# Kernel optimization log

Hardware: AMD Instinct MI355X
Metric: run time of the kernel (lower is better)

The kernel has to match this reference:

```python
import jax, jax.numpy as jnp
import numpy as np

B, S, E, H, R = 512, 50, 128, 8, 32
D = E // H  # depth per head
USERS, ITEMS, ALLSEQ, NCLASS = 50000, 20000, 20000, 5


def setup_inputs() -> dict:
    key = jax.random.key(0)
    ks = jax.random.split(key, 20)
    n = lambda k, shp, s=0.05: jax.random.normal(k, shp, dtype=jnp.float32) * s
    return {
        "user": jax.random.randint(ks[0], (B,), 0, USERS),
        "item": jax.random.randint(ks[1], (B,), 0, ITEMS),
        "neighbor": jax.random.randint(ks[2], (B, S), 0, USERS),
        "seq": jax.random.randint(ks[3], (B, S), 0, ALLSEQ),
        "user_emb_table": n(ks[4], (USERS, E)),
        "item_emb_table": n(ks[5], (ITEMS, E)),
        "user_item_LCU": n(ks[6], (ALLSEQ, R, E), 0.01),
        "item_user_LCU": n(ks[7], (ALLSEQ, R, E), 0.01),
        "wq": n(ks[8], (E, E)), "bq": jnp.zeros((E,), jnp.float32),
        "wk": n(ks[9], (E, E)), "bk": jnp.zeros((E,), jnp.float32),
        "wv": n(ks[10], (E, E)), "bv": jnp.zeros((E,), jnp.float32),
        "wo": n(ks[11], (E, E)), "bo": jnp.zeros((E,), jnp.float32),
        "fc_w": n(ks[12], (R, NCLASS)), "fc_b": jnp.zeros((NCLASS,), jnp.float32),
    }


def _forward(user, item, neighbor, seq,
             user_emb_table, item_emb_table, user_item_LCU, item_user_LCU,
             wq, bq, wk, bk, wv, bv, wo, bo, fc_w, fc_b):
    user_emb = user_emb_table[user]            # [B,E]
    neighbor_emb = user_emb_table[neighbor]    # [B,S,E]
    item_emb = item_emb_table[item]            # [B,E]
    weight = (neighbor > 0).astype(jnp.float32)  # [B,S] padding mask (1=real)

    # ---- single-query multi-head attention (use_attention=True) ----
    q = (user_emb @ wq + bq).reshape(B, H, D)                       # [B,H,D]
    k = (neighbor_emb @ wk + bk).reshape(B, S, H, D).transpose(0, 2, 1, 3)  # [B,H,S,D]
    v = (neighbor_emb @ wv + bv).reshape(B, S, H, D).transpose(0, 2, 1, 3)  # [B,H,S,D]
    logits = jnp.einsum('bhd,bhsd->bhs', q, k) / jnp.sqrt(jnp.float32(D))
    logits = logits + (1.0 - weight)[:, None, :] * (-1e9)           # mask padding
    attn = jax.nn.softmax(logits, axis=-1)                          # [B,H,S]
    ctx = attn[..., None] * v                                       # [B,H,S,D]
    ctx = ctx.transpose(0, 2, 1, 3).reshape(B, S, E)                # [B,S,E]
    neighbor_emb = ctx @ wo + bo                                    # [B,S,E]

    # ---- region embedding ----
    K_ui = user_item_LCU[seq]   # [B,S,R,E]
    K_iu = item_user_LCU[seq]   # [B,S,R,E]
    neighbor_profile = jnp.einsum('bsre,bse->bsr', K_iu, neighbor_emb)  # [B,S,R]
    item_profile = jnp.einsum('bsre,be->bsr', K_ui, item_emb)          # [B,S,R]
    neighbor_rating = neighbor_profile * item_profile * weight[:, :, None]
    user_rating_vector = jnp.max(neighbor_rating, axis=1)              # [B,R]

    # ---- rating classifier ----
    return jax.nn.softmax(user_rating_vector @ fc_w + fc_b, axis=-1)   # [B,NCLASS]


def reference(user, item, neighbor, seq,
              user_emb_table, item_emb_table, user_item_LCU, item_user_LCU,
              wq, bq, wk, bk, wv, bv, wo, bo, fc_w, fc_b):
    return _forward(user, item, neighbor, seq,
                    user_emb_table, item_emb_table, user_item_LCU, item_user_LCU,
                    wq, bq, wk, bk, wv, bv, wo, bo, fc_w, fc_b)
```

## Files before the change

### kernel.cpp

```cpp
#include <hip/hip_runtime.h>
#include <math.h>

#define BB 512
#define SS 50
#define EE 128
#define HH 8
#define RR 32
#define NC 5
#define NSEQ 20000
#define NBS (BB*SS)
#define LDK 136
#define NRB 2048

typedef __attribute__((ext_vector_type(8))) __bf16 bf16x8;
typedef __attribute__((ext_vector_type(4))) float f32x4;
typedef __attribute__((ext_vector_type(4))) unsigned short us4;

__device__ __forceinline__ unsigned short f2bf(float f) {
    unsigned int u = __float_as_uint(f);
    unsigned int r = (u + 0x7fffu + ((u >> 16) & 1u)) >> 16;
    return (unsigned short)r;
}
__device__ __forceinline__ float dot4v(const f32x4& a, const float4& b) {
    return a[0]*b.x + a[1]*b.y + a[2]*b.z + a[3]*b.w;
}

__global__ __launch_bounds__(256) void prep_kernel(const float* __restrict__ wv,
                                                   const float* __restrict__ wo,
                                                   unsigned short* __restrict__ wvT,
                                                   unsigned short* __restrict__ woT,
                                                   const int* __restrict__ seq,
                                                   int* __restrict__ hist) {
    const int bid = blockIdx.x, t = threadIdx.x;
    if (bid < 128) {
        const int n = bid;
        if (t < 128) wvT[n*EE + t] = f2bf(wv[t*EE + n]);
        else         woT[n*EE + (t - 128)] = f2bf(wo[(t - 128)*EE + n]);
    } else {
        const int i = (bid - 128) * 256 + t;
        if (i < NBS) atomicAdd(&hist[seq[i]], 1);
    }
}

__global__ __launch_bounds__(1024) void scan_kernel(int* __restrict__ hist,
                                                    int* __restrict__ jlist,
                                                    int* __restrict__ jstart,
                                                    int* __restrict__ Mcount) {
    const int t = threadIdx.x;
    const int CH = 20;
    const int base = t * CH;
    int val[CH];
    int s = 0, cz = 0;
    #pragma unroll
    for (int i = 0; i < CH; ++i) {
        int idx = base + i;
        int v = (idx < NSEQ) ? hist[idx] : 0;
        val[i] = v;
        s += v;
        cz += (v > 0) ? 1 : 0;
    }
    const int lane = t & 63, w = t >> 6;
    int incl = s, incl2 = cz;
    #pragma unroll
    for (int off = 1; off < 64; off <<= 1) {
        int n1 = __shfl_up(incl, off);
        int n2 = __shfl_up(incl2, off);
        if (lane >= off) { incl += n1; incl2 += n2; }
    }
    __shared__ int wsum[16], wsum2[16];
    if (lane == 63) { wsum[w] = incl; wsum2[w] = incl2; }
    __syncthreads();
    if (t == 0) {
        int a = 0, b = 0;
        #pragma unroll
        for (int k = 0; k < 16; ++k) {
            int v1 = wsum[k], v2 = wsum2[k];
            wsum[k] = a; wsum2[k] = b;
            a += v1; b += v2;
        }
    }
    __syncthreads();
    int e  = incl  - s  + wsum[w];
    int c2 = incl2 - cz + wsum2[w];
    #pragma unroll
    for (int i = 0; i < CH; ++i) {
        int idx = base + i;
        if (idx < NSEQ) {
            hist[idx] = e;
            if (val[i] > 0) { jlist[c2] = idx; jstart[c2] = e; ++c2; }
            e += val[i];
        }
    }
    if (t == 1023) {
        int M = wsum2[15] + incl2;
        Mcount[0] = M;
        jstart[M] = NBS;
    }
}

__global__ __launch_bounds__(256) void scatter_kernel(const int* __restrict__ seq,
                                                      const int* __restrict__ neighbor,
                                                      const int* __restrict__ item,
                                                      int* __restrict__ hist,
                                                      int* __restrict__ pinfo,
                                                      int* __restrict__ pitem) {
    int i = blockIdx.x * 256 + threadIdx.x;
    if (i < NBS) {
        int pos = atomicAdd(&hist[seq[i]], 1);
        pinfo[pos] = i | ((neighbor[i] > 0) ? 0 : 0x80000000);
        pitem[pos] = item[(unsigned)i / SS];
    }
}

__global__ __launch_bounds__(256, 4) void attn_kernel(
    const int* __restrict__ user,
    const int* __restrict__ neighbor,
    const float* __restrict__ uet,
    const float* __restrict__ wq, const float* __restrict__ bq,
    const float* __restrict__ wk, const float* __restrict__ bk,
    const float* __restrict__ bv, const float* __restrict__ bo,
    const unsigned short* __restrict__ wvT, const unsigned short* __restrict__ woT,
    float* __restrict__ ws_ne2)
{
    __shared__ unsigned short kA[64*LDK];
    __shared__ unsigned short qkvT[16][EE];
    __shared__ float ue[EE];
    __shared__ float qs[EE];
    __shared__ float qkb[HH];
    __shared__ float attn_s[HH][64];
    __shared__ float maskadd[64];

    const int b = blockIdx.x;
    const int t = threadIdx.x;

    if (t < EE) ue[t] = uet[(size_t)user[b]*EE + t];
    if (t < 64) maskadd[t] = (t < SS && neighbor[b*SS + t] > 0) ? 0.f : -1e9f;
    for (int idx = t; idx < SS*32; idx += 256) {
        int s = idx >> 5, g = idx & 31;
        float4 v = ((const float4*)(uet + (size_t)neighbor[b*SS + s]*EE))[g];
        us4 o; o.x = f2bf(v.x); o.y = f2bf(v.y); o.z = f2bf(v.z); o.w = f2bf(v.w);
        *(us4*)&kA[s*LDK + g*4] = o;
    }
    for (int idx = t; idx < 14*LDK; idx += 256) kA[50*LDK + idx] = 0;
    for (int idx = t; idx < 8*EE; idx += 256) qkvT[8 + (idx >> 7)][idx & 127] = 0;
    __syncthreads();

    if (t < EE) {
        float acc = bq[t];
        #pragma unroll 4
        for (int e = 0; e < EE; ++e) acc = fmaf(ue[e], wq[e*EE + t], acc);
        qs[t] = acc;
    }
    __syncthreads();

    {
        const int e = t >> 1, h0 = (t & 1) * 4;
        const float* wrow = wk + e*EE;
        #pragma unroll
        for (int j = 0; j < 4; ++j) {
            int h = h0 + j;
            float acc = 0.f;
            #pragma unroll
            for (int d = 0; d < 16; ++d) acc = fmaf(qs[h*16 + d], wrow[h*16 + d], acc);
            qkvT[h][e] = f2bf(acc);
        }
    }
    if (t < HH) {
        float acc = 0.f;
        #pragma unroll
        for (int d = 0; d < 16; ++d) acc = fmaf(qs[t*16 + d], bk[t*16 + d], acc);
        qkb[t] = acc;
    }
    __syncthreads();

    const int w    = t >> 6;
    const int l    = t & 63;
    const int lrow = l & 15;
    const int kg   = l >> 4;

    bf16x8 a0 = *(const bf16x8*)&kA[(w*16 + lrow)*LDK +  0 + kg*8];
    bf16x8 a1 = *(const bf16x8*)&kA[(w*16 + lrow)*LDK + 32 + kg*8];
    bf16x8 a2 = *(const bf16x8*)&kA[(w*16 + lrow)*LDK + 64 + kg*8];
    bf16x8 a3 = *(const bf16x8*)&kA[(w*16 + lrow)*LDK + 96 + kg*8];

    {
        bf16x8 b0 = *(const bf16x8*)&qkvT[lrow][ 0 + kg*8];
        bf16x8 b1 = *(const bf16x8*)&qkvT[lrow][32 + kg*8];
        bf16x8 b2 = *(const bf16x8*)&qkvT[lrow][64 + kg*8];
        bf16x8 b3 = *(const bf16x8*)&qkvT[lrow][96 + kg*8];
        f32x4 c = {0.f, 0.f, 0.f, 0.f};
        c = __builtin_amdgcn_mfma_f32_16x16x32_bf16(a0, b0, c, 0, 0, 0);
        c = __builtin_amdgcn_mfma_f32_16x16x32_bf16(a1, b1, c, 0, 0, 0);
        c = __builtin_amdgcn_mfma_f32_16x16x32_bf16(a2, b2, c, 0, 0, 0);
        c = __builtin_amdgcn_mfma_f32_16x16x32_bf16(a3, b3, c, 0, 0, 0);
        const int h = lrow;
        if (h < HH) {
            #pragma unroll
            for (int rg = 0; rg < 4; ++rg) {
                const int row = w*16 + kg*4 + rg;
                attn_s[h][row] = (c[rg] + qkb[h]) * 0.25f + maskadd[row];
            }
        }
    }
    __syncthreads();

    if (t < 64) {
        int h = t >> 3, ll = t & 7;
        float mx = -3e38f;
        #pragma unroll
        for (int i = 0; i < 7; ++i) { int s = i*8 + ll; if (s < SS) mx = fmaxf(mx, attn_s[h][s]); }
        mx = fmaxf(mx, __shfl_xor(mx, 1));
        mx = fmaxf(mx, __shfl_xor(mx, 2));
        mx = fmaxf(mx, __shfl_xor(mx, 4));
        float ev[7]; float sm_ = 0.f;
        #pragma unroll
        for (int i = 0; i < 7; ++i) {
            int s = i*8 + ll; ev[i] = 0.f;
            if (s < SS) { ev[i] = expf(attn_s[h][s] - mx); sm_ += ev[i]; }
        }
        sm_ += __shfl_xor(sm_, 1);
        sm_ += __shfl_xor(sm_, 2);
        sm_ += __shfl_xor(sm_, 4);
        float inv = 1.f / sm_;
        #pragma unroll
        for (int i = 0; i < 7; ++i) { int s = i*8 + ll; if (s < SS) attn_s[h][s] = ev[i] * inv; }
    }
    __syncthreads();

    f32x4 acc[8];
    #pragma unroll
    for (int nt = 0; nt < 8; ++nt) {
        const unsigned short* bp = wvT + (nt*16 + lrow)*EE + kg*8;
        bf16x8 b0 = *(const bf16x8*)&bp[0];
        bf16x8 b1 = *(const bf16x8*)&bp[32];
        bf16x8 b2 = *(const bf16x8*)&bp[64];
        bf16x8 b3 = *(const bf16x8*)&bp[96];
        f32x4 c = {0.f, 0.f, 0.f, 0.f};
        c = __builtin_amdgcn_mfma_f32_16x16x32_bf16(a0, b0, c, 0, 0, 0);
        c = __builtin_amdgcn_mfma_f32_16x16x32_bf16(a1, b1, c, 0, 0, 0);
        c = __builtin_amdgcn_mfma_f32_16x16x32_bf16(a2, b2, c, 0, 0, 0);
        c = __builtin_amdgcn_mfma_f32_16x16x32_bf16(a3, b3, c, 0, 0, 0);
        acc[nt] = c;
    }
    #pragma unroll
    for (int nt = 0; nt < 8; ++nt) {
        const int col = nt*16 + lrow;
        const float bvc = bv[col];
        #pragma unroll
        for (int rg = 0; rg < 4; ++rg) {
            const int row = w*16 + kg*4 + rg;
            const float av = (row < SS) ? attn_s[nt][row] : 0.f;
            kA[row*LDK + col] = f2bf((acc[nt][rg] + bvc) * av);
        }
    }
    __syncthreads();

    bf16x8 c0 = *(const bf16x8*)&kA[(w*16 + lrow)*LDK +  0 + kg*8];
    bf16x8 c1 = *(const bf16x8*)&kA[(w*16 + lrow)*LDK + 32 + kg*8];
    bf16x8 c2 = *(const bf16x8*)&kA[(w*16 + lrow)*LDK + 64 + kg*8];
    bf16x8 c3 = *(const bf16x8*)&kA[(w*16 + lrow)*LDK + 96 + kg*8];

    #pragma unroll
    for (int nt = 0; nt < 8; ++nt) {
        const unsigned short* bp = woT + (nt*16 + lrow)*EE + kg*8;
        bf16x8 b0 = *(const bf16x8*)&bp[0];
        bf16x8 b1 = *(const bf16x8*)&bp[32];
        bf16x8 b2 = *(const bf16x8*)&bp[64];
        bf16x8 b3 = *(const bf16x8*)&bp[96];
        f32x4 c = {0.f, 0.f, 0.f, 0.f};
        c = __builtin_amdgcn_mfma_f32_16x16x32_bf16(c0, b0, c, 0, 0, 0);
        c = __builtin_amdgcn_mfma_f32_16x16x32_bf16(c1, b1, c, 0, 0, 0);
        c = __builtin_amdgcn_mfma_f32_16x16x32_bf16(c2, b2, c, 0, 0, 0);
        c = __builtin_amdgcn_mfma_f32_16x16x32_bf16(c3, b3, c, 0, 0, 0);
        const int col = nt*16 + lrow;
        const float boc = bo[col];
        #pragma unroll
        for (int rg = 0; rg < 4; ++rg) {
            const int row = w*16 + kg*4 + rg;
            if (row < SS)
                ws_ne2[((size_t)b*SS + row)*EE + col] = c[rg] + boc;
        }
    }
}

__global__ __launch_bounds__(256) void region_kernel(
    const float* __restrict__ iu_lcu, const float* __restrict__ ui_lcu,
    const float* __restrict__ ws_ne2, const float* __restrict__ iet,
    const int* __restrict__ jlist, const int* __restrict__ jstart,
    const int* __restrict__ pinfo, const int* __restrict__ pitem,
    const int* __restrict__ Mcount,
    float* __restrict__ ws_np, float* __restrict__ ws_ip)
{
    const int M = Mcount[0];
    const int half = blockIdx.x >> 11;
    int c = blockIdx.x & (NRB - 1);
    if (c >= M) return;

    const int t = threadIdx.x, r = t >> 3, l = t & 7;
    const float* lcu  = half ? ui_lcu : iu_lcu;
    const float* vecs = half ? iet    : ws_ne2;
    float* outb       = half ? ws_ip  : ws_np;

    f32x4 A0, A1, A2, A3, B0, B1, B2, B3;
    int sCur, eCur;
    {
        int j = jlist[c];
        sCur = jstart[c]; eCur = jstart[c+1];
        const f32x4* kp = (const f32x4*)(lcu + ((size_t)j*RR + r)*EE);
        A0 = kp[l]; A1 = kp[l+8]; A2 = kp[l+16]; A3 = kp[l+24];
    }

#define DOTSTORE(P0,P1,P2,P3, v0,v1,v2,v3, info_) {                               \
    float acc_ = dot4v(P0,v0) + dot4v(P1,v1) + dot4v(P2,v2) + dot4v(P3,v3);       \
    acc_ += __shfl_xor(acc_,1); acc_ += __shfl_xor(acc_,2); acc_ += __shfl_xor(acc_,4); \
    if (l == 0) {                                                                 \
        int bs_ = (info_) & 0xFFFF;                                               \
        outb[(size_t)bs_*RR + r] = half ? acc_ : (((info_) < 0) ? 0.f : acc_);    \
    } }

#define STAGE(C0,C1,C2,C3, N0,N1,N2,N3) {                                         \
    const int sC = sCur, eC = eCur, nC = eC - sC;                                 \
    const int cn = c + NRB;                                                       \
    const bool more = (cn < M);                                                   \
    const int jN = more ? jlist[cn] : 0;                                          \
    sCur = more ? jstart[cn]   : 0;                                               \
    eCur = more ? jstart[cn+1] : 0;                                               \
    const int i0 = pinfo[sC];                                                     \
    const int i1 = (nC >= 2) ? pinfo[sC+1] : i0;                                  \
    const int t0 = half ? pitem[sC] : (i0 & 0xFFFF);                              \
    const int t1 = half ? ((nC >= 2) ? pitem[sC+1] : t0) : (i1 & 0xFFFF);         \
    const float4* rb0 = (const float4*)(vecs + (size_t)t0*EE);                    \
    float4 r0 = rb0[l], r1 = rb0[l+8], r2 = rb0[l+16], r3 = rb0[l+24];            \
    float4 s0, s1, s2, s3;                                                        \
    if (nC >= 2) {                                                                \
        const float4* rb1 = (const float4*)(vecs + (size_t)t1*EE);                \
        s0 = rb1[l]; s1 = rb1[l+8]; s2 = rb1[l+16]; s3 = rb1[l+24];               \
    }                                                                             \
    if (more) {                                                                   \
        const f32x4* kp = (const f32x4*)(lcu + ((size_t)jN*RR + r)*EE);           \
        N0 = kp[l]; N1 = kp[l+8]; N2 = kp[l+16]; N3 = kp[l+24];                   \
    }                                                                             \
    DOTSTORE(C0,C1,C2,C3, r0,r1,r2,r3, i0);                                       \
    if (nC >= 2) DOTSTORE(C0,C1,C2,C3, s0,s1,s2,s3, i1);                          \
    for (int o = sC + 2; o < eC; ++o) {                                           \
        const int ii = pinfo[o];                                                  \
        const int tt = half ? pitem[o] : (ii & 0xFFFF);                           \
        const float4* rb = (const float4*)(vecs + (size_t)tt*EE);                 \
        float4 q0 = rb[l], q1 = rb[l+8], q2 = rb[l+16], q3 = rb[l+24];            \
        DOTSTORE(C0,C1,C2,C3, q0,q1,q2,q3, ii);                                   \
    }                                                                             \
    if (!more) break;                                                             \
    c = cn; }

    while (true) {
        STAGE(A0,A1,A2,A3, B0,B1,B2,B3)
        STAGE(B0,B1,B2,B3, A0,A1,A2,A3)
    }
#undef STAGE
#undef DOTSTORE
}

__global__ __launch_bounds__(256) void head_kernel(
    const float* __restrict__ ws_np, const float* __restrict__ ws_ip,
    const float* __restrict__ fc_w, const float* __restrict__ fc_b,
    float* __restrict__ out)
{
    __shared__ float part[8][RR];
    __shared__ float urv[RR];
    __shared__ float lg[NC];
    const int b = blockIdx.x, t = threadIdx.x;
    const int r = t & 31, sub = t >> 5;

    float m = -3e38f;
    for (int s = sub; s < SS; s += 8) {
        const size_t idx = ((size_t)b*SS + s)*RR + r;
        m = fmaxf(m, ws_np[idx] * ws_ip[idx]);
    }
    part[sub][r] = m;
    __syncthreads();
    if (t < RR) {
        float mm = part[0][t];
        #pragma unroll
        for (int k = 1; k < 8; ++k) mm = fmaxf(mm, part[k][t]);
        urv[t] = mm;
    }
    __syncthreads();
    if (t < NC) {
        float acc = fc_b[t];
        #pragma unroll
        for (int rr = 0; rr < RR; ++rr) acc = fmaf(urv[rr], fc_w[rr*NC + t], acc);
        lg[t] = acc;
    }
    __syncthreads();
    if (t < NC) {
        float mx = lg[0];
        #pragma unroll
        for (int cc = 1; cc < NC; ++cc) mx = fmaxf(mx, lg[cc]);
        float sm = 0.f;
        #pragma unroll
        for (int cc = 0; cc < NC; ++cc) sm += expf(lg[cc] - mx);
        out[b*NC + t] = expf(lg[t] - mx) / sm;
    }
}

extern "C" void kernel_launch(void* const* d_in, const int* in_sizes, int n_in,
                              void* d_out, int out_size, void* d_ws, size_t ws_size,
                              hipStream_t stream) {
    const int*   user     = (const int*)d_in[0];
    const int*   item     = (const int*)d_in[1];
    const int*   neighbor = (const int*)d_in[2];
    const int*   seq      = (const int*)d_in[3];
    const float* uet      = (const float*)d_in[4];
    const float* iet      = (const float*)d_in[5];
    const float* ui_lcu   = (const float*)d_in[6];
    const float* iu_lcu   = (const float*)d_in[7];
    const float* wq = (const float*)d_in[8];   const float* bq = (const float*)d_in[9];
    const float* wk = (const float*)d_in[10];  const float* bk = (const float*)d_in[11];
    const float* wv = (const float*)d_in[12];  const float* bv = (const float*)d_in[13];
    const float* wo = (const float*)d_in[14];  const float* bo = (const float*)d_in[15];
    const float* fcw = (const float*)d_in[16]; const float* fcb = (const float*)d_in[17];

    float* ws = (float*)d_ws;
    float* ws_ne2 = ws;
    float* ws_np  = ws_ne2 + (size_t)BB*SS*EE;
    float* ws_ip  = ws_np  + (size_t)BB*SS*RR;
    unsigned short* wvT = (unsigned short*)(ws_ip + (size_t)BB*SS*RR);
    unsigned short* woT = wvT + EE*EE;
    int* hist   = (int*)(woT + EE*EE);
    int* jlist  = hist + NSEQ;
    int* jstart = jlist + NSEQ;
    int* Mcount = jstart + NSEQ + 1;
    int* pinfo  = Mcount + 1;
    int* pitem  = pinfo + NBS;
    float* out = (float*)d_out;

    hipMemsetAsync(hist, 0, NSEQ * sizeof(int), stream);
    hipLaunchKernelGGL(prep_kernel, dim3(128 + (NBS + 255)/256), dim3(256), 0, stream,
                       wv, wo, wvT, woT, seq, hist);
    hipLaunchKernelGGL(scan_kernel, dim3(1), dim3(1024), 0, stream,
                       hist, jlist, jstart, Mcount);
    hipLaunchKernelGGL(scatter_kernel, dim3((NBS + 255)/256), dim3(256), 0, stream,
                       seq, neighbor, item, hist, pinfo, pitem);

    hipLaunchKernelGGL(attn_kernel, dim3(BB), dim3(256), 0, stream,
                       user, neighbor, uet,
                       wq, bq, wk, bk, bv, bo, wvT, woT, ws_ne2);

    hipLaunchKernelGGL(region_kernel, dim3(2*NRB), dim3(256), 0, stream,
                       iu_lcu, ui_lcu, ws_ne2, iet,
                       jlist, jstart, pinfo, pitem, Mcount, ws_np, ws_ip);

    hipLaunchKernelGGL(head_kernel, dim3(BB), dim3(256), 0, stream,
                       ws_np, ws_ip, fcw, fcb, out);
}
```

Measured before the change: 195.1 us.

## Pre-gather region vectors into contiguous buffers and launch one block per sequence

Adds a gather kernel that copies each occurrence's neighbor-context and item embedding rows into contiguous buffers in sorted occurrence order. The region kernel then streams those rows sequentially with one-ahead prefetch, and launches one block per distinct sequence id instead of a persistent 2048-block loop with cross-stage LCU prefetch. This is meant to replace scattered indirect row loads with contiguous reads and to raise parallelism. In exchange it adds a 25600-block launch and writes and reads about 26 MB of extra intermediate data, plus up to 40000 blocks that may mostly exit early.

After: 204.1 us. 1.05x slower.

```diff
diff --git a/kernel.cpp b/kernel.cpp
--- a/kernel.cpp
+++ b/kernel.cpp
@@ -10,7 +10,6 @@
 #define NSEQ 20000
 #define NBS (BB*SS)
 #define LDK 136
-#define NRB 2048
 
 typedef __attribute__((ext_vector_type(8))) __bf16 bf16x8;
 typedef __attribute__((ext_vector_type(4))) float f32x4;
@@ -21,8 +20,8 @@
     unsigned int r = (u + 0x7fffu + ((u >> 16) & 1u)) >> 16;
     return (unsigned short)r;
 }
-__device__ __forceinline__ float dot4v(const f32x4& a, const float4& b) {
-    return a[0]*b.x + a[1]*b.y + a[2]*b.z + a[3]*b.w;
+__device__ __forceinline__ float dot44(const f32x4& a, const f32x4& b) {
+    return a[0]*b[0] + a[1]*b[1] + a[2]*b[2] + a[3]*b[3];
 }
 
 __global__ __launch_bounds__(256) void prep_kernel(const float* __restrict__ wv,
@@ -283,81 +282,63 @@
     }
 }
 
+__global__ __launch_bounds__(256) void gather_kernel(
+    const float* __restrict__ ws_ne2, const float* __restrict__ iet,
+    const int* __restrict__ pinfo, const int* __restrict__ pitem,
+    float* __restrict__ rhs_np, float* __restrict__ rhs_ip)
+{
+    const int o = blockIdx.x;
+    const int t = threadIdx.x;
+    if (t < 128) {
+        const int info = pinfo[o];
+        const int bs = info & 0xFFFF;
+        rhs_np[(size_t)o*EE + t] = (info < 0) ? 0.f : ws_ne2[(size_t)bs*EE + t];
+    } else {
+        rhs_ip[(size_t)o*EE + (t - 128)] = iet[(size_t)pitem[o]*EE + (t - 128)];
+    }
+}
+
 __global__ __launch_bounds__(256) void region_kernel(
     const float* __restrict__ iu_lcu, const float* __restrict__ ui_lcu,
-    const float* __restrict__ ws_ne2, const float* __restrict__ iet,
+    const float* __restrict__ rhs_np, const float* __restrict__ rhs_ip,
     const int* __restrict__ jlist, const int* __restrict__ jstart,
-    const int* __restrict__ pinfo, const int* __restrict__ pitem,
-    const int* __restrict__ Mcount,
+    const int* __restrict__ pinfo, const int* __restrict__ Mcount,
     float* __restrict__ ws_np, float* __restrict__ ws_ip)
 {
     const int M = Mcount[0];
-    const int half = blockIdx.x >> 11;
-    int c = blockIdx.x & (NRB - 1);
+    const bool ip = (blockIdx.x >= NSEQ);
+    const int c = ip ? (blockIdx.x - NSEQ) : blockIdx.x;
     if (c >= M) return;
 
     const int t = threadIdx.x, r = t >> 3, l = t & 7;
-    const float* lcu  = half ? ui_lcu : iu_lcu;
-    const float* vecs = half ? iet    : ws_ne2;
-    float* outb       = half ? ws_ip  : ws_np;
-
-    f32x4 A0, A1, A2, A3, B0, B1, B2, B3;
-    int sCur, eCur;
-    {
-        int j = jlist[c];
-        sCur = jstart[c]; eCur = jstart[c+1];
-        const f32x4* kp = (const f32x4*)(lcu + ((size_t)j*RR + r)*EE);
-        A0 = kp[l]; A1 = kp[l+8]; A2 = kp[l+16]; A3 = kp[l+24];
-    }
-
-#define DOTSTORE(P0,P1,P2,P3, v0,v1,v2,v3, info_) {                               \
-    float acc_ = dot4v(P0,v0) + dot4v(P1,v1) + dot4v(P2,v2) + dot4v(P3,v3);       \
-    acc_ += __shfl_xor(acc_,1); acc_ += __shfl_xor(acc_,2); acc_ += __shfl_xor(acc_,4); \
-    if (l == 0) {                                                                 \
-        int bs_ = (info_) & 0xFFFF;                                               \
-        outb[(size_t)bs_*RR + r] = half ? acc_ : (((info_) < 0) ? 0.f : acc_);    \
-    } }
-
-#define STAGE(C0,C1,C2,C3, N0,N1,N2,N3) {                                         \
-    const int sC = sCur, eC = eCur, nC = eC - sC;                                 \
-    const int cn = c + NRB;                                                       \
-    const bool more = (cn < M);                                                   \
-    const int jN = more ? jlist[cn] : 0;                                          \
-    sCur = more ? jstart[cn]   : 0;                                               \
-    eCur = more ? jstart[cn+1] : 0;                                               \
-    const int i0 = pinfo[sC];                                                     \
-    const int i1 = (nC >= 2) ? pinfo[sC+1] : i0;                                  \
-    const int t0 = half ? pitem[sC] : (i0 & 0xFFFF);                              \
-    const int t1 = half ? ((nC >= 2) ? pitem[sC+1] : t0) : (i1 & 0xFFFF);         \
-    const float4* rb0 = (const float4*)(vecs + (size_t)t0*EE);                    \
-    float4 r0 = rb0[l], r1 = rb0[l+8], r2 = rb0[l+16], r3 = rb0[l+24];            \
-    float4 s0, s1, s2, s3;                                                        \
-    if (nC >= 2) {                                                                \
-        const float4* rb1 = (const float4*)(vecs + (size_t)t1*EE);                \
-        s0 = rb1[l]; s1 = rb1[l+8]; s2 = rb1[l+16]; s3 = rb1[l+24];               \
-    }                                                                             \
-    if (more) {                                                                   \
-        const f32x4* kp = (const f32x4*)(lcu + ((size_t)jN*RR + r)*EE);           \
-        N0 = kp[l]; N1 = kp[l+8]; N2 = kp[l+16]; N3 = kp[l+24];                   \
-    }                                                                             \
-    DOTSTORE(C0,C1,C2,C3, r0,r1,r2,r3, i0);                                       \
-    if (nC >= 2) DOTSTORE(C0,C1,C2,C3, s0,s1,s2,s3, i1);                          \
-    for (int o = sC + 2; o < eC; ++o) {                                           \
-        const int ii = pinfo[o];                                                  \
-        const int tt = half ? pitem[o] : (ii & 0xFFFF);                           \
-        const float4* rb = (const float4*)(vecs + (size_t)tt*EE);                 \
-        float4 q0 = rb[l], q1 = rb[l+8], q2 = rb[l+16], q3 = rb[l+24];            \
-        DOTSTORE(C0,C1,C2,C3, q0,q1,q2,q3, ii);                                   \
-    }                                                                             \
-    if (!more) break;                                                             \
-    c = cn; }
-
-    while (true) {
-        STAGE(A0,A1,A2,A3, B0,B1,B2,B3)
-        STAGE(B0,B1,B2,B3, A0,A1,A2,A3)
-    }
-#undef STAGE
-#undef DOTSTORE
+    const float* lcu = ip ? ui_lcu : iu_lcu;
+    const float* rhs = ip ? rhs_ip : rhs_np;
+    float* outb      = ip ? ws_ip  : ws_np;
+
+    const int j  = jlist[c];
+    const int s0 = jstart[c], s1 = jstart[c + 1];
+
+    const f32x4* kp = (const f32x4*)(lcu + ((size_t)j*RR + r)*EE);
+    f32x4 P0 = kp[l], P1 = kp[l+8], P2 = kp[l+16], P3 = kp[l+24];
+
+    const f32x4* rp = (const f32x4*)(rhs + (size_t)s0*EE);
+    f32x4 R0 = rp[l], R1 = rp[l+8], R2 = rp[l+16], R3 = rp[l+24];
+
+    for (int o = s0; o < s1; ++o) {
+        f32x4 N0, N1, N2, N3;
+        const bool more = (o + 1 < s1);
+        if (more) {
+            const f32x4* q = (const f32x4*)(rhs + (size_t)(o + 1)*EE);
+            N0 = q[l]; N1 = q[l+8]; N2 = q[l+16]; N3 = q[l+24];
+        }
+        float acc = dot44(P0, R0) + dot44(P1, R1) + dot44(P2, R2) + dot44(P3, R3);
+        acc += __shfl_xor(acc, 1); acc += __shfl_xor(acc, 2); acc += __shfl_xor(acc, 4);
+        if (l == 0) {
+            const int bs = pinfo[o] & 0xFFFF;
+            outb[(size_t)bs*RR + r] = acc;
+        }
+        if (more) { R0 = N0; R1 = N1; R2 = N2; R3 = N3; }
+    }
 }
 
 __global__ __launch_bounds__(256) void head_kernel(
@@ -423,8 +404,10 @@
     float* ws = (float*)d_ws;
     float* ws_ne2 = ws;
     float* ws_np  = ws_ne2 + (size_t)BB*SS*EE;
-    float* ws_ip  = ws_np  + (size_t)BB*SS*RR;
-    unsigned short* wvT = (unsigned short*)(ws_ip + (size_t)BB*SS*RR);
+    float* ws_ip  = ws_np  + (size_t)NBS*RR;
+    float* rhs_np = ws_ip  + (size_t)NBS*RR;
+    float* rhs_ip = rhs_np + (size_t)NBS*EE;
+    unsigned short* wvT = (unsigned short*)(rhs_ip + (size_t)NBS*EE);
     unsigned short* woT = wvT + EE*EE;
     int* hist   = (int*)(woT + EE*EE);
     int* jlist  = hist + NSEQ;
@@ -446,9 +429,12 @@
                        user, neighbor, uet,
                        wq, bq, wk, bk, bv, bo, wvT, woT, ws_ne2);
 
-    hipLaunchKernelGGL(region_kernel, dim3(2*NRB), dim3(256), 0, stream,
-                       iu_lcu, ui_lcu, ws_ne2, iet,
-                       jlist, jstart, pinfo, pitem, Mcount, ws_np, ws_ip);
+    hipLaunchKernelGGL(gather_kernel, dim3(NBS), dim3(256), 0, stream,
+                       ws_ne2, iet, pinfo, pitem, rhs_np, rhs_ip);
+
+    hipLaunchKernelGGL(region_kernel, dim3(2*NSEQ), dim3(256), 0, stream,
+                       iu_lcu, ui_lcu, rhs_np, rhs_ip,
+                       jlist, jstart, pinfo, Mcount, ws_np, ws_ip);
 
     hipLaunchKernelGGL(head_kernel, dim3(BB), dim3(256), 0, stream,
                        ws_np, ws_ip, fcw, fcb, out);
```
